# Kernel optimization log

Hardware: AMD Instinct MI355X
Metric: run time of the kernel (lower is better)

Reference implementation:

```python
import jax, jax.numpy as jnp
import numpy as np

H = 16      # num_heads
DK = 128    # head_dim_qk
DV = 128    # head_dim_v
HID = 2048  # hidden_size
KS = 4      # conv kernel size


def _causal_dwconv(x, w, b):
    # x: [B, T, C], w: [C, KS], b: [C] -- depthwise causal conv (torch pads KS-1 then slices [:T])
    xc = jnp.transpose(x, (0, 2, 1))  # [B, C, T]
    out = jax.lax.conv_general_dilated(
        xc, w[:, None, :], window_strides=(1,), padding=[(KS - 1, 0)],
        feature_group_count=xc.shape[1], dimension_numbers=('NCH', 'OIH', 'NCH'))
    out = out + b[None, :, None]
    return jnp.transpose(out, (0, 2, 1))


def setup_inputs() -> dict:
    key = jax.random.key(0)
    ks = jax.random.split(key, 16)
    s = 0.02
    inp = {
        'x':   jax.random.normal(ks[0], (4, 2048, HID), jnp.float32),
        'Wq':  jax.random.normal(ks[1], (HID, H * DK), jnp.float32) * s,
        'Wk':  jax.random.normal(ks[2], (HID, H * DK), jnp.float32) * s,
        'Wv':  jax.random.normal(ks[3], (HID, H * DV), jnp.float32) * s,
        'Wa':  jax.random.normal(ks[4], (HID, H), jnp.float32) * s,
        'ba':  jnp.zeros((H,), jnp.float32),
        'Wb':  jax.random.normal(ks[5], (HID, H), jnp.float32) * s,
        'bb':  jnp.zeros((H,), jnp.float32),
        'Wg':  jax.random.normal(ks[6], (HID, H * DV), jnp.float32) * s,
        'Wo':  jax.random.normal(ks[7], (H * DV, HID), jnp.float32) * s,
        'qcw': jax.random.normal(ks[8], (H * DK, KS), jnp.float32) * 0.3,
        'qcb': jnp.zeros((H * DK,), jnp.float32),
        'kcw': jax.random.normal(ks[9], (H * DK, KS), jnp.float32) * 0.3,
        'kcb': jnp.zeros((H * DK,), jnp.float32),
        'vcw': jax.random.normal(ks[10], (H * DV, KS), jnp.float32) * 0.3,
        'vcb': jnp.zeros((H * DV,), jnp.float32),
        'ln_w': jnp.ones((DV,), jnp.float32),
        'ln_b': jnp.zeros((DV,), jnp.float32),
    }
    return inp


def _forward(x, Wq, Wk, Wv, Wa, ba, Wb, bb, Wg, Wo, qcw, qcb, kcw, kcb, vcw, vcb, ln_w, ln_b):
    B, T, _ = x.shape
    q = jax.nn.silu(_causal_dwconv(x @ Wq, qcw, qcb))
    k = jax.nn.silu(_causal_dwconv(x @ Wk, kcw, kcb))
    v = jax.nn.silu(_causal_dwconv(x @ Wv, vcw, vcb))
    q = q.reshape(B, T, H, DK)
    k = k.reshape(B, T, H, DK) * (DK ** -0.5)
    v = v.reshape(B, T, H, DV)
    alpha = jax.nn.sigmoid(x @ Wa + ba)  # [B, T, H]
    beta = jax.nn.sigmoid(x @ Wb + bb)   # [B, T, H]

    # time-major for scan
    qT = jnp.transpose(q, (1, 0, 2, 3))
    kT = jnp.transpose(k, (1, 0, 2, 3))
    vT = jnp.transpose(v, (1, 0, 2, 3))
    aT = jnp.transpose(alpha, (1, 0, 2))
    bT = jnp.transpose(beta, (1, 0, 2))

    def step(S, inps):
        qt, kt, vt, at, bt = inps
        Sk = jnp.einsum('bhvk,bhk->bhv', S, kt)            # S @ k
        err = Sk - vt
        S = at[..., None, None] * S - bt[..., None, None] * (err[..., None] * kt[:, :, None, :])
        ot = jnp.einsum('bhvk,bhk->bhv', S, qt)            # output uses NEW state
        return S, ot

    S0 = jnp.zeros((B, H, DV, DK), x.dtype)
    _, oT = jax.lax.scan(step, S0, (qT, kT, vT, aT, bT))    # [T, B, H, DV]
    o = jnp.transpose(oT, (1, 0, 2, 3))                      # [B, T, H, DV]

    # LayerNorm over head_dim_v (eps=1e-5)
    mu = jnp.mean(o, axis=-1, keepdims=True)
    var = jnp.mean(jnp.square(o - mu), axis=-1, keepdims=True)
    o = (o - mu) * jax.lax.rsqrt(var + 1e-5) * ln_w + ln_b

    g = jax.nn.sigmoid(x @ Wg).reshape(B, T, H, DV)
    o = (o * g).reshape(B, T, H * DV)
    return o @ Wo


def reference(x, Wq, Wk, Wv, Wa, ba, Wb, bb, Wg, Wo, qcw, qcb, kcw, kcb, vcw, vcb, ln_w, ln_b):
    return _forward(x, Wq, Wk, Wv, Wa, ba, Wb, bb, Wg, Wo, qcw, qcb, kcw, kcb, vcw, vcb, ln_w, ln_b)
```

## Files before the change

### kernel.cpp

```cpp
#include <hip/hip_runtime.h>
#include <stdint.h>

#define H_   16
#define DK_  128
#define DV_  128
#define HID_ 2048
#define KS_  4
#define B_   4
#define T_   2048
#define BT_  (B_*T_)
#define QKVC (3*HID_)
#define C_   32
#define RS_  32

typedef unsigned short u16;
typedef short  bf16x8 __attribute__((ext_vector_type(8)));
typedef u16    u16x8  __attribute__((ext_vector_type(8)));
typedef u16    u16x4  __attribute__((ext_vector_type(4)));
typedef float  f32x4  __attribute__((ext_vector_type(4)));

__device__ __forceinline__ float b2f(u16 u){
  union { unsigned int i; float f; } v; v.i = ((unsigned int)u) << 16; return v.f;
}
__device__ __forceinline__ u16 f2b(float f){
  unsigned int x = __float_as_uint(f);
  unsigned int r = (x + 0x7FFFu + ((x >> 16) & 1u)) >> 16;
  return (u16)r;
}
__device__ __forceinline__ float sigm(float x){ return 1.0f / (1.0f + __expf(-x)); }

#define MFMA16(a,b,c) __builtin_amdgcn_mfma_f32_16x16x32_bf16((a),(b),(c),0,0,0)

__global__ __launch_bounds__(256) void cvt_x_k(const f32x4* __restrict__ src,
                                               u16x4* __restrict__ dst, int n4)
{
  int i0 = blockIdx.x * 256 + threadIdx.x;
  int stride = gridDim.x * 256;
  for (int i = i0; i < n4; i += stride) {
    f32x4 v = src[i];
    u16x4 r; r[0] = f2b(v[0]); r[1] = f2b(v[1]); r[2] = f2b(v[2]); r[3] = f2b(v[3]);
    dst[i] = r;
  }
}

__global__ __launch_bounds__(256) void cvt_small_k(
    const float* __restrict__ qcw, const float* __restrict__ kcw, const float* __restrict__ vcw,
    const float* __restrict__ qcb, const float* __restrict__ kcb, const float* __restrict__ vcb,
    const float* __restrict__ ba,  const float* __restrict__ bb,
    const float* __restrict__ lnw, const float* __restrict__ lnb,
    u16* __restrict__ canon)
{
  int i = blockIdx.x * 256 + threadIdx.x;
  if (i >= 31008) return;
  float v;
  if (i < 24576) {
    const float* s = (i < 8192) ? qcw : (i < 16384) ? kcw : vcw;
    v = s[i & 8191];
  } else if (i < 30720) {
    int j = i - 24576;
    const float* s = (j < 2048) ? qcb : (j < 4096) ? kcb : vcb;
    v = s[j & 2047];
  } else if (i < 30752) {
    int j = i - 30720;
    v = (j < 16) ? ba[j] : bb[j - 16];
  } else {
    int j = i - 30752;
    v = (j < 128) ? lnw[j] : lnb[j - 128];
  }
  canon[i] = f2b(v);
}

__global__ __launch_bounds__(256) void transpose_b(const float* __restrict__ s0,
                                                   const float* __restrict__ s1,
                                                   const float* __restrict__ s2,
                                                   u16* __restrict__ dst,
                                                   int R, int C)
{
  int z = blockIdx.z;
  const float* src = (z == 0) ? s0 : (z == 1) ? s1 : s2;
  u16* d = dst + (size_t)z * R * C;
  __shared__ u16 t[32][33];
  int bx = blockIdx.x * 32;
  int by = blockIdx.y * 32;
  int lx = threadIdx.x & 31, ly = threadIdx.x >> 5;
  #pragma unroll
  for (int i = 0; i < 4; ++i) {
    int r = by + ly + i * 8, c = bx + lx;
    if (r < R && c < C) t[ly + i * 8][lx] = f2b(src[(size_t)r * C + c]);
  }
  __syncthreads();
  #pragma unroll
  for (int i = 0; i < 4; ++i) {
    int r = bx + ly + i * 8;
    int c = by + lx;
    if (r < C && c < R) d[(size_t)r * R + c] = t[lx][ly + i * 8];
  }
}

#define BM 128
#define BN 128
#define BK 32

__device__ __forceinline__ void gload_lds16(const void* gp, void* lp){
  __builtin_amdgcn_global_load_lds(
      (const __attribute__((address_space(1))) void*)gp,
      (__attribute__((address_space(3))) void*)lp, 16, 0, 0);
}

__global__ __launch_bounds__(256) void gemm_bt(const u16* __restrict__ A, int lda,
                                               const u16* __restrict__ Bt, int ldb,
                                               void* __restrict__ C, int ldc,
                                               int K, int out_f32)
{
  __shared__ u16 lsA[BM * BK];
  __shared__ u16 lsB[BN * BK];
  int tid = threadIdx.x, wave = tid >> 6, lane = tid & 63;
  int m0 = blockIdx.y * BM, n0 = blockIdx.x * BN;
  int wm = (wave >> 1) * 64, wn = (wave & 1) * 64;
  int srow = lane >> 2;
  int skel = (lane & 3) * 8;
  int quad = lane >> 4, l16 = lane & 15;

  f32x4 acc[4][4];
  #pragma unroll
  for (int mi = 0; mi < 4; ++mi)
    #pragma unroll
    for (int ni = 0; ni < 4; ++ni)
      #pragma unroll
      for (int r = 0; r < 4; ++r) acc[mi][ni][r] = 0.0f;

  for (int k0 = 0; k0 < K; k0 += BK) {
    __syncthreads();
    #pragma unroll
    for (int i = 0; i < 2; ++i) {
      int row = wave * 32 + i * 16 + srow;
      gload_lds16(A  + (size_t)(m0 + row) * lda + k0 + skel,
                  lsA + (wave * 2048 + i * 1024) / 2);
      gload_lds16(Bt + (size_t)(n0 + row) * ldb + k0 + skel,
                  lsB + (wave * 2048 + i * 1024) / 2);
    }
    __syncthreads();

    const bf16x8* fA = (const bf16x8*)lsA;
    const bf16x8* fB = (const bf16x8*)lsB;
    bf16x8 af[4], bg[4];
    #pragma unroll
    for (int mi = 0; mi < 4; ++mi) af[mi] = fA[(wm + mi * 16 + l16) * 4 + quad];
    #pragma unroll
    for (int ni = 0; ni < 4; ++ni) bg[ni] = fB[(wn + ni * 16 + l16) * 4 + quad];
    #pragma unroll
    for (int mi = 0; mi < 4; ++mi)
      #pragma unroll
      for (int ni = 0; ni < 4; ++ni)
        acc[mi][ni] = MFMA16(af[mi], bg[ni], acc[mi][ni]);
  }

  #pragma unroll
  for (int mi = 0; mi < 4; ++mi)
    #pragma unroll
    for (int ni = 0; ni < 4; ++ni)
      #pragma unroll
      for (int r = 0; r < 4; ++r) {
        int m = m0 + wm + mi * 16 + quad * 4 + r;
        int n = n0 + wn + ni * 16 + l16;
        if (out_f32) ((float*)C)[(size_t)m * ldc + n] = acc[mi][ni][r];
        else         ((u16*)C)[(size_t)m * ldc + n] = f2b(acc[mi][ni][r]);
      }
}

__global__ __launch_bounds__(256) void ab_k(const u16* __restrict__ x,
                                            const u16* __restrict__ WabT,
                                            const u16* __restrict__ ba,
                                            const u16* __restrict__ bb,
                                            float* __restrict__ ab)
{
  int j = threadIdx.x & 31, rl = threadIdx.x >> 5;
  int row = blockIdx.x * 8 + rl;
  const u16x8* xr = (const u16x8*)(x + (size_t)row * HID_);
  const u16x8* wr = (const u16x8*)(WabT + (size_t)j * HID_);
  float acc = 0.f;
  for (int k = 0; k < HID_ / 8; ++k) {
    u16x8 xv = xr[k], wv = wr[k];
    #pragma unroll
    for (int i = 0; i < 8; ++i) acc += b2f(xv[i]) * b2f(wv[i]);
  }
  float bias = (j < 16) ? b2f(ba[j]) : b2f(bb[j - 16]);
  float sg = sigm(acc + bias);
  if (j < 16) ab[(size_t)row * 16 + j] = sg;
  else        ab[(size_t)BT_ * 16 + (size_t)row * 16 + (j - 16)] = sg;
}

__global__ __launch_bounds__(256) void conv_silu_k(const u16* __restrict__ in,
                                                   const u16* __restrict__ cwv,
                                                   const u16* __restrict__ cbv,
                                                   u16* __restrict__ out)
{
  int idx  = blockIdx.x * 256 + threadIdx.x;
  int col8 = idx % (QKVC / 8);
  int t    = idx / (QKVC / 8);
  int col  = col8 * 8;
  int s = col >> 11;

  u16 wl[32];
  #pragma unroll
  for (int i = 0; i < 4; ++i)
    *(u16x8*)(wl + i * 8) = *(const u16x8*)(cwv + (size_t)col * KS_ + i * 8);
  u16x8 bv = *(const u16x8*)(cbv + col);

  float acc[8];
  #pragma unroll
  for (int j = 0; j < 8; ++j) acc[j] = b2f(bv[j]);

  #pragma unroll
  for (int tap = 0; tap < KS_; ++tap) {
    int tt = t - 3 + tap;
    if (tt >= 0) {
      u16x8 xv = *(const u16x8*)(in + (size_t)tt * QKVC + col);
      #pragma unroll
      for (int j = 0; j < 8; ++j) acc[j] = fmaf(b2f(xv[j]), b2f(wl[j * 4 + tap]), acc[j]);
    }
  }
  float scale = (s == 1) ? 0.08838834764831845f : 1.0f;
  u16x8 rv;
  #pragma unroll
  for (int j = 0; j < 8; ++j) {
    float a = acc[j];
    rv[j] = f2b(a * sigm(a) * scale);
  }
  *(u16x8*)(out + (size_t)t * QKVC + col) = rv;
}

__global__ __launch_bounds__(256) void chunk_scan_k(const u16* __restrict__ qkv,
                                                    const float* __restrict__ ab,
                                                    u16* __restrict__ o)
{
  __shared__ __align__(16) char smem[64000];
  u16 (*Kim)[136]  = (u16(*)[136])(smem);
  u16 (*Qim)[136]  = (u16(*)[136])(smem + 8704);
  u16 (*Sh)[136]   = (u16(*)[136])(smem + 17408);
  u16 (*Sl)[136]   = (u16(*)[136])(smem + 26112);
  u16 (*KT)[40]    = (u16(*)[40])(smem + 34816);
  u16 (*Vim)[32]   = (u16(*)[32])(smem + 45056);
  float (*KK)[32]  = (float(*)[32])(smem + 47104);
  float (*KQ)[32]  = (float(*)[32])(smem + 51200);
  float (*SK0)[32] = (float(*)[32])(smem + 55296);
  float (*SQ0)[32] = (float(*)[32])(smem + 59392);
  float (*PL4)[4]  = (float(*)[4])(smem + 63488);
  float (*U)[32]   = (float(*)[32])(smem + 8704);
  u16 (*Gh)[40]  = (u16(*)[40])(smem + 17408);
  u16 (*Gl)[40]  = (u16(*)[40])(smem + 19968);
  u16 (*Uch)[40] = (u16(*)[40])(smem + 22528);
  u16 (*Ucl)[40] = (u16(*)[40])(smem + 25088);
  u16 (*Uth)[40] = (u16(*)[40])(smem + 27648);
  u16 (*Utl)[40] = (u16(*)[40])(smem + 30208);

  int bid = blockIdx.x;
  int chain = bid & 63, rblk = bid >> 6;
  int b = chain >> 4, h = chain & 15;
  int tid = threadIdx.x, wv = tid >> 6, lane = tid & 63;
  int l16 = lane & 15, quad = lane >> 4;

  const u16* kbase = qkv + (size_t)b * T_ * QKVC + HID_ + h * DK_;
  const u16* qbase = qkv + (size_t)b * T_ * QKVC + h * DK_;
  const u16* vbase = qkv + (size_t)b * T_ * QKVC + 2 * HID_ + h * DV_ + rblk * RS_;
  const float* abase = ab + (size_t)b * T_ * 16 + h;
  const float* bbase = abase + (size_t)BT_ * 16;
  u16* obase = o + (size_t)b * T_ * 2048 + h * DV_ + rblk * RS_;

  f32x4 st[2][2];
  #pragma unroll
  for (int rt = 0; rt < 2; ++rt)
    #pragma unroll
    for (int ct = 0; ct < 2; ++ct)
      #pragma unroll
      for (int r = 0; r < 4; ++r) st[rt][ct][r] = 0.f;

  for (int c = 0; c < T_ / C_; ++c) {
    int t0 = c * C_;

    #pragma unroll
    for (int rt = 0; rt < 2; ++rt)
      #pragma unroll
      for (int ct = 0; ct < 2; ++ct)
        #pragma unroll
        for (int r = 0; r < 4; ++r) {
          float s = st[rt][ct][r];
          u16 hi = f2b(s);
          float lo = s - b2f(hi);
          int row = rt * 16 + quad * 4 + r;
          int col = wv * 32 + ct * 16 + l16;
          Sh[row][col] = hi;
          Sl[row][col] = f2b(lo);
        }

    if (wv == 0) {
      float av = (lane < 32) ? abase[(size_t)(t0 + lane) * 16]
                             : bbase[(size_t)(t0 + lane - 32) * 16];
      float p = av;
      #pragma unroll
      for (int d = 1; d < 32; d <<= 1) {
        float up = __shfl_up(p, d);
        if (lane >= d && lane < 32) p *= up;
      }
      float pm1 = __shfl_up(p, 1);
      float bt = __shfl(av, lane + 32);
      if (lane < 32) {
        if (lane == 0) pm1 = 1.f;
        f32x4 g;
        g[0] = bt * pm1;
        g[1] = bt;
        g[2] = 1.0f / p;
        g[3] = p;
        *(f32x4*)PL4[lane] = g;
      }
    } else {
      u16x8 tmp[6];
      int jb = tid - 64;
      #pragma unroll
      for (int it = 0; it < 6; ++it) {
        int j = jb + it * 192;
        if (j < 512) {
          int t = j >> 4, g = j & 15;
          tmp[it] = *(const u16x8*)(kbase + (size_t)(t0 + t) * QKVC + g * 8);
        } else if (j < 1024) {
          int j2 = j - 512; int t = j2 >> 4, g = j2 & 15;
          tmp[it] = *(const u16x8*)(qbase + (size_t)(t0 + t) * QKVC + g * 8);
        } else {
          int j2 = j - 1024; int t = j2 >> 2, rg = j2 & 3;
          tmp[it] = *(const u16x8*)(vbase + (size_t)(t0 + t) * QKVC + rg * 8);
        }
      }
      #pragma unroll
      for (int it = 0; it < 6; ++it) {
        int j = jb + it * 192;
        if (j < 512) {
          int t = j >> 4, g = j & 15;
          *(u16x8*)&Kim[t][g * 8] = tmp[it];
          #pragma unroll
          for (int e = 0; e < 8; ++e) KT[g * 8 + e][t] = tmp[it][e];
        } else if (j < 1024) {
          int j2 = j - 512; int t = j2 >> 4, g = j2 & 15;
          *(u16x8*)&Qim[t][g * 8] = tmp[it];
        } else {
          int j2 = j - 1024; int t = j2 >> 2, rg = j2 & 3;
          *(u16x8*)&Vim[t][rg * 8] = tmp[it];
        }
      }
    }
    __syncthreads();

    {
      int mt = wv >> 1, nt = wv & 1;
      f32x4 aKK = {0.f,0.f,0.f,0.f}, aKQ = {0.f,0.f,0.f,0.f};
      f32x4 aSK = {0.f,0.f,0.f,0.f}, aSQ = {0.f,0.f,0.f,0.f};
      #pragma unroll
      for (int ks = 0; ks < 4; ++ks) {
        bf16x8 Ak  = *(const bf16x8*)&Kim[mt * 16 + l16][ks * 32 + quad * 8];
        bf16x8 Aq  = *(const bf16x8*)&Qim[mt * 16 + l16][ks * 32 + quad * 8];
        bf16x8 Bk  = *(const bf16x8*)&Kim[nt * 16 + l16][ks * 32 + quad * 8];
        bf16x8 Bsh = *(const bf16x8*)&Sh[nt * 16 + l16][ks * 32 + quad * 8];
        bf16x8 Bsl = *(const bf16x8*)&Sl[nt * 16 + l16][ks * 32 + quad * 8];
        aKK = MFMA16(Ak, Bk, aKK);
        aKQ = MFMA16(Aq, Bk, aKQ);
        aSK = MFMA16(Ak, Bsh, aSK);
        aSK = MFMA16(Ak, Bsl, aSK);
        aSQ = MFMA16(Aq, Bsh, aSQ);
        aSQ = MFMA16(Aq, Bsl, aSQ);
      }
      #pragma unroll
      for (int r = 0; r < 4; ++r) {
        int m = mt * 16 + quad * 4 + r, n = nt * 16 + l16;
        KK[m][n] = aKK[r]; KQ[m][n] = aKQ[r];
        SK0[m][n] = aSK[r]; SQ0[m][n] = aSQ[r];
      }
    }
    __syncthreads();

    if (wv == 0 && lane < 32) {
      float ub[C_];
      #pragma unroll
      for (int t = 0; t < C_; ++t) {
        f32x4 g = *(const f32x4*)PL4[t];
        float u = g[0] * SK0[t][lane] - g[1] * b2f(Vim[t][lane]);
        float acc = 0.f;
        #pragma unroll
        for (int i = 0; i < t; ++i) acc = fmaf(KK[t][i], ub[i], acc);
        u = fmaf(-g[0], acc, u);
        U[t][lane] = u;
        ub[t] = g[2] * u;
      }
    }
    __syncthreads();

    {
      float PL31 = PL4[31][3];
      int row = tid & 31, i0 = (tid >> 5) * 4;
      #pragma unroll
      for (int ii = 0; ii < 4; ++ii) {
        int i = i0 + ii;
        float rPi = PL4[i][2];
        float uv = U[i][row];
        u16 h1 = f2b(uv);
        Uth[row][i] = h1; Utl[row][i] = f2b(uv - b2f(h1));
        float ucv = -PL31 * rPi * uv;
        u16 h2 = f2b(ucv);
        Uch[row][i] = h2; Ucl[row][i] = f2b(ucv - b2f(h2));
        float gv = (i <= row) ? (-PL4[row][3] * rPi * KQ[row][i]) : 0.f;
        u16 h3 = f2b(gv);
        Gh[row][i] = h3; Gl[row][i] = f2b(gv - b2f(h3));
      }
    }
    __syncthreads();

    {
      float PL31 = PL4[31][3];
      #pragma unroll
      for (int rt = 0; rt < 2; ++rt) {
        bf16x8 Ah = *(const bf16x8*)&Uch[rt * 16 + l16][quad * 8];
        bf16x8 Al = *(const bf16x8*)&Ucl[rt * 16 + l16][quad * 8];
        #pragma unroll
        for (int ct = 0; ct < 2; ++ct) {
          bf16x8 Bk = *(const bf16x8*)&KT[wv * 32 + ct * 16 + l16][quad * 8];
          f32x4 cacc;
          #pragma unroll
          for (int r = 0; r < 4; ++r) cacc[r] = PL31 * st[rt][ct][r];
          cacc = MFMA16(Ah, Bk, cacc);
          cacc = MFMA16(Al, Bk, cacc);
          st[rt][ct] = cacc;
        }
      }
      int mt = wv >> 1, nt = wv & 1;
      bf16x8 Agh = *(const bf16x8*)&Gh[mt * 16 + l16][quad * 8];
      bf16x8 Agl = *(const bf16x8*)&Gl[mt * 16 + l16][quad * 8];
      bf16x8 Buh = *(const bf16x8*)&Uth[nt * 16 + l16][quad * 8];
      bf16x8 Bul = *(const bf16x8*)&Utl[nt * 16 + l16][quad * 8];
      f32x4 oacc;
      #pragma unroll
      for (int r = 0; r < 4; ++r) {
        int t = mt * 16 + quad * 4 + r;
        oacc[r] = PL4[t][3] * SQ0[t][nt * 16 + l16];
      }
      oacc = MFMA16(Agh, Buh, oacc);
      oacc = MFMA16(Agh, Bul, oacc);
      oacc = MFMA16(Agl, Buh, oacc);
      #pragma unroll
      for (int r = 0; r < 4; ++r) {
        int t = mt * 16 + quad * 4 + r;
        obase[(size_t)(t0 + t) * 2048 + nt * 16 + l16] = f2b(oacc[r]);
      }
    }
    __syncthreads();
  }
}

__global__ __launch_bounds__(256) void ln_gate_k(const u16* __restrict__ o_raw,
                                                 const u16* __restrict__ g,
                                                 const u16* __restrict__ lnw,
                                                 const u16* __restrict__ lnb,
                                                 u16* __restrict__ o_ln)
{
  int gid = blockIdx.x * 4 + (threadIdx.x >> 6);
  int lane = threadIdx.x & 63;
  int row = gid >> 4, h = gid & 15;
  size_t ofs = (size_t)row * 2048 + h * 128 + lane * 2;
  unsigned int e2 = *(const unsigned int*)(o_raw + ofs);
  float ex = b2f((u16)(e2 & 0xffff)), ey = b2f((u16)(e2 >> 16));
  float s = ex + ey, ss = ex * ex + ey * ey;
  #pragma unroll
  for (int m = 1; m < 64; m <<= 1) { s += __shfl_xor(s, m); ss += __shfl_xor(ss, m); }
  float mean = s * (1.f / 128.f);
  float var  = ss * (1.f / 128.f) - mean * mean;
  float rstd = rsqrtf(fmaxf(var, 0.f) + 1e-5f);
  float w0 = b2f(lnw[lane * 2]), w1 = b2f(lnw[lane * 2 + 1]);
  float b0 = b2f(lnb[lane * 2]), b1 = b2f(lnb[lane * 2 + 1]);
  unsigned int g2 = *(const unsigned int*)(g + ofs);
  float g0 = sigm(b2f((u16)(g2 & 0xffff))), g1 = sigm(b2f((u16)(g2 >> 16)));
  float r0 = ((ex - mean) * rstd * w0 + b0) * g0;
  float r1 = ((ey - mean) * rstd * w1 + b1) * g1;
  *(unsigned int*)(o_ln + ofs) = (unsigned int)f2b(r0) | ((unsigned int)f2b(r1) << 16);
}

extern "C" void kernel_launch(void* const* d_in, const int* in_sizes, int n_in,
                              void* d_out, int out_size, void* d_ws, size_t ws_size,
                              hipStream_t stream)
{
  const float* x   = (const float*)d_in[0];
  const float* Wq  = (const float*)d_in[1];
  const float* Wk  = (const float*)d_in[2];
  const float* Wv  = (const float*)d_in[3];
  const float* Wa  = (const float*)d_in[4];
  const float* ba  = (const float*)d_in[5];
  const float* Wb  = (const float*)d_in[6];
  const float* bb  = (const float*)d_in[7];
  const float* Wg  = (const float*)d_in[8];
  const float* Wo  = (const float*)d_in[9];
  const float* qcw = (const float*)d_in[10];
  const float* qcb = (const float*)d_in[11];
  const float* kcw = (const float*)d_in[12];
  const float* kcb = (const float*)d_in[13];
  const float* vcw = (const float*)d_in[14];
  const float* vcb = (const float*)d_in[15];
  const float* lnw = (const float*)d_in[16];
  const float* lnb = (const float*)d_in[17];
  (void)in_sizes; (void)n_in; (void)out_size;

  char* ws = (char*)d_ws;
  size_t off = 0;
  auto alloc = [&](size_t bytes) -> void* {
    void* p = ws + off; off += (bytes + 255) & ~(size_t)255; return p;
  };
  u16* WT    = (u16*)alloc((size_t)3 * HID_ * HID_ * 2);
  u16* WabT  = (u16*)alloc((size_t)32 * HID_ * 2);
  u16* xc    = (u16*)alloc((size_t)BT_ * HID_ * 2);
  u16* canon = (u16*)alloc((size_t)31008 * 2);
  u16* preC  = (u16*)alloc((size_t)BT_ * HID_ * 2 * 2);
  u16* post  = (u16*)alloc((size_t)BT_ * QKVC * 2);
  float* abuf = (float*)alloc((size_t)2 * BT_ * 16 * 4);
  if (off > ws_size) return;

  u16* cw_c  = canon;
  u16* cb_c  = canon + 24576;
  u16* ba_c  = canon + 30720;
  u16* bb_c  = canon + 30736;
  u16* lnw_c = canon + 30752;
  u16* lnb_c = canon + 30880;

  u16* o_raw = preC;
  u16* g_raw = post;
  u16* o_ln  = post + (size_t)BT_ * HID_;
  u16* WTg   = WT;

  dim3 tb(256);

  cvt_x_k<<<dim3(4096), tb, 0, stream>>>((const f32x4*)x, (u16x4*)xc, BT_ * HID_ / 4);
  cvt_small_k<<<dim3(122), tb, 0, stream>>>(qcw, kcw, vcw, qcb, kcb, vcb, ba, bb, lnw, lnb, canon);

  transpose_b<<<dim3(64, 64, 3), tb, 0, stream>>>(Wq, Wk, Wv, WT, HID_, HID_);
  transpose_b<<<dim3(1, 64, 2), tb, 0, stream>>>(Wa, Wb, Wb, WabT, HID_, 16);

  for (int b = 0; b < B_; ++b) {
    const u16* xb = xc + (size_t)b * T_ * HID_;
    gemm_bt<<<dim3(QKVC / BN, T_ / BM), tb, 0, stream>>>(xb, HID_, WT, HID_, preC, QKVC, HID_, 0);
    conv_silu_k<<<dim3(T_ * (QKVC / 8) / 256), tb, 0, stream>>>(
        preC, cw_c, cb_c, post + (size_t)b * T_ * QKVC);
  }

  transpose_b<<<dim3(64, 64, 2), tb, 0, stream>>>(Wg, Wo, Wo, WTg, HID_, HID_);

  ab_k<<<dim3(BT_ / 8), tb, 0, stream>>>(xc, WabT, ba_c, bb_c, abuf);

  chunk_scan_k<<<dim3(256), tb, 0, stream>>>(post, abuf, o_raw);

  gemm_bt<<<dim3(HID_ / BN, BT_ / BM), tb, 0, stream>>>(xc, HID_, WTg, HID_, g_raw, HID_, HID_, 0);

  ln_gate_k<<<dim3(BT_ * H_ / 4), tb, 0, stream>>>(o_raw, g_raw, lnw_c, lnb_c, o_ln);

  gemm_bt<<<dim3(HID_ / BN, BT_ / BM), tb, 0, stream>>>(o_ln, HID_,
      WT + (size_t)HID_ * HID_, HID_, d_out, HID_, HID_, 1);
}
```

Measured before the change: 1.387 ms.

## Split chunk-scan state rows across more blocks and prefetch next chunk

The chunk-scan kernel now gives each block 16 value rows instead of 32, so twice as many blocks (512) run, and shared memory per block shrinks. The next chunk's K/Q/V/alpha-beta loads are issued into registers before the compute of the current chunk, overlapping global latency with work. Intra-chunk matmuls are redistributed by wave, with KK computed only for lower-triangular tiles, G-matrix construction moved into the otherwise idle waves during the sequential solve, and an XOR swizzle added to the K-transpose buffer to cut bank conflicts. The cost is that the KK/KQ and K/Q loads are now repeated in twice as many blocks.

```diff
diff --git a/kernel.cpp b/kernel.cpp
--- a/kernel.cpp
+++ b/kernel.cpp
@@ -11,7 +11,8 @@
 #define BT_  (B_*T_)
 #define QKVC (3*HID_)
 #define C_   32
-#define RS_  32
+#define RS_  16
+#define NC_  (T_/C_)
 
 typedef unsigned short u16;
 typedef short  bf16x8 __attribute__((ext_vector_type(8)));
@@ -234,25 +235,25 @@
                                                     const float* __restrict__ ab,
                                                     u16* __restrict__ o)
 {
-  __shared__ __align__(16) char smem[64000];
+  __shared__ __align__(16) char smem[50688];
   u16 (*Kim)[136]  = (u16(*)[136])(smem);
   u16 (*Qim)[136]  = (u16(*)[136])(smem + 8704);
   u16 (*Sh)[136]   = (u16(*)[136])(smem + 17408);
-  u16 (*Sl)[136]   = (u16(*)[136])(smem + 26112);
-  u16 (*KT)[40]    = (u16(*)[40])(smem + 34816);
-  u16 (*Vim)[32]   = (u16(*)[32])(smem + 45056);
-  float (*KK)[32]  = (float(*)[32])(smem + 47104);
-  float (*KQ)[32]  = (float(*)[32])(smem + 51200);
-  float (*SK0)[32] = (float(*)[32])(smem + 55296);
-  float (*SQ0)[32] = (float(*)[32])(smem + 59392);
-  float (*PL4)[4]  = (float(*)[4])(smem + 63488);
-  float (*U)[32]   = (float(*)[32])(smem + 8704);
-  u16 (*Gh)[40]  = (u16(*)[40])(smem + 17408);
-  u16 (*Gl)[40]  = (u16(*)[40])(smem + 19968);
-  u16 (*Uch)[40] = (u16(*)[40])(smem + 22528);
-  u16 (*Ucl)[40] = (u16(*)[40])(smem + 25088);
-  u16 (*Uth)[40] = (u16(*)[40])(smem + 27648);
-  u16 (*Utl)[40] = (u16(*)[40])(smem + 30208);
+  u16 (*Sl)[136]   = (u16(*)[136])(smem + 21760);
+  u16 (*KT)[40]    = (u16(*)[40])(smem + 26112);
+  u16 (*Vim)[16]   = (u16(*)[16])(smem + 36352);
+  float (*KK)[33]  = (float(*)[33])(smem + 37376);
+  float (*KQ)[33]  = (float(*)[33])(smem + 41600);
+  float (*SK0)[17] = (float(*)[17])(smem + 45824);
+  float (*SQ0)[17] = (float(*)[17])(smem + 48000);
+  float (*PL4)[4]  = (float(*)[4])(smem + 50176);
+  float (*U)[17]   = (float(*)[17])(smem + 8704);
+  u16 (*Uth)[40]   = (u16(*)[40])(smem + 10880);
+  u16 (*Utl)[40]   = (u16(*)[40])(smem + 12160);
+  u16 (*Uch)[40]   = (u16(*)[40])(smem + 13440);
+  u16 (*Ucl)[40]   = (u16(*)[40])(smem + 14720);
+  u16 (*Gh)[40]    = (u16(*)[40])(smem + 17408);
+  u16 (*Gl)[40]    = (u16(*)[40])(smem + 21760);
 
   int bid = blockIdx.x;
   int chain = bid & 63, rblk = bid >> 6;
@@ -267,35 +268,59 @@
   const float* bbase = abase + (size_t)BT_ * 16;
   u16* obase = o + (size_t)b * T_ * 2048 + h * DV_ + rblk * RS_;
 
-  f32x4 st[2][2];
-  #pragma unroll
-  for (int rt = 0; rt < 2; ++rt)
+  f32x4 st[2];
+  #pragma unroll
+  for (int ct = 0; ct < 2; ++ct)
+    #pragma unroll
+    for (int r = 0; r < 4; ++r) st[ct][r] = 0.f;
+
+  int jb = tid - 64;
+  u16x8 stg[6];
+  float avp = 0.f;
+
+  auto LD = [&](int c) {
+    int t0 = c * C_;
+    if (wv == 0) {
+      avp = (lane < 32) ? abase[(size_t)(t0 + lane) * 16]
+                        : bbase[(size_t)(t0 + lane - 32) * 16];
+    } else {
+      #pragma unroll
+      for (int it = 0; it < 6; ++it) {
+        int j = jb + it * 192;
+        if (j < 512) {
+          int t = j >> 4, g = j & 15;
+          stg[it] = *(const u16x8*)(kbase + (size_t)(t0 + t) * QKVC + g * 8);
+        } else if (j < 1024) {
+          int j2 = j - 512, t = j2 >> 4, g = j2 & 15;
+          stg[it] = *(const u16x8*)(qbase + (size_t)(t0 + t) * QKVC + g * 8);
+        } else if (j < 1088) {
+          int j2 = j - 1024, t = j2 >> 1, rg = j2 & 1;
+          stg[it] = *(const u16x8*)(vbase + (size_t)(t0 + t) * QKVC + rg * 8);
+        }
+      }
+    }
+  };
+
+  LD(0);
+
+  for (int c = 0; c < NC_; ++c) {
+    int t0 = c * C_;
+
     #pragma unroll
     for (int ct = 0; ct < 2; ++ct)
       #pragma unroll
-      for (int r = 0; r < 4; ++r) st[rt][ct][r] = 0.f;
-
-  for (int c = 0; c < T_ / C_; ++c) {
-    int t0 = c * C_;
-
-    #pragma unroll
-    for (int rt = 0; rt < 2; ++rt)
-      #pragma unroll
-      for (int ct = 0; ct < 2; ++ct)
-        #pragma unroll
-        for (int r = 0; r < 4; ++r) {
-          float s = st[rt][ct][r];
-          u16 hi = f2b(s);
-          float lo = s - b2f(hi);
-          int row = rt * 16 + quad * 4 + r;
-          int col = wv * 32 + ct * 16 + l16;
-          Sh[row][col] = hi;
-          Sl[row][col] = f2b(lo);
-        }
+      for (int r = 0; r < 4; ++r) {
+        float s = st[ct][r];
+        u16 hi = f2b(s);
+        float lo = s - b2f(hi);
+        int row = quad * 4 + r;
+        int col = wv * 32 + ct * 16 + l16;
+        Sh[row][col] = hi;
+        Sl[row][col] = f2b(lo);
+      }
 
     if (wv == 0) {
-      float av = (lane < 32) ? abase[(size_t)(t0 + lane) * 16]
-                             : bbase[(size_t)(t0 + lane - 32) * 16];
+      float av = avp;
       float p = av;
       #pragma unroll
       for (int d = 1; d < 32; d <<= 1) {
@@ -307,146 +332,173 @@
       if (lane < 32) {
         if (lane == 0) pm1 = 1.f;
         f32x4 g;
-        g[0] = bt * pm1;
-        g[1] = bt;
-        g[2] = 1.0f / p;
-        g[3] = p;
+        g[0] = bt * pm1; g[1] = bt; g[2] = 1.0f / p; g[3] = p;
         *(f32x4*)PL4[lane] = g;
       }
     } else {
-      u16x8 tmp[6];
-      int jb = tid - 64;
       #pragma unroll
       for (int it = 0; it < 6; ++it) {
         int j = jb + it * 192;
         if (j < 512) {
           int t = j >> 4, g = j & 15;
-          tmp[it] = *(const u16x8*)(kbase + (size_t)(t0 + t) * QKVC + g * 8);
+          *(u16x8*)&Kim[t][g * 8] = stg[it];
+          int tb = t >> 3, tl = t & 7;
+          int blk = (tb ^ (g & 3)) << 3;
+          #pragma unroll
+          for (int e = 0; e < 8; ++e)
+            KT[g * 8 + e][blk + tl] = stg[it][e];
         } else if (j < 1024) {
-          int j2 = j - 512; int t = j2 >> 4, g = j2 & 15;
-          tmp[it] = *(const u16x8*)(qbase + (size_t)(t0 + t) * QKVC + g * 8);
-        } else {
-          int j2 = j - 1024; int t = j2 >> 2, rg = j2 & 3;
-          tmp[it] = *(const u16x8*)(vbase + (size_t)(t0 + t) * QKVC + rg * 8);
-        }
-      }
+          int j2 = j - 512, t = j2 >> 4, g = j2 & 15;
+          *(u16x8*)&Qim[t][g * 8] = stg[it];
+        } else if (j < 1088) {
+          int j2 = j - 1024, t = j2 >> 1, rg = j2 & 1;
+          *(u16x8*)&Vim[t][rg * 8] = stg[it];
+        }
+      }
+    }
+    if (c + 1 < NC_) LD(c + 1);
+    __syncthreads();
+
+    if (wv == 0) {
+      #pragma unroll
+      for (int mt = 0; mt < 2; ++mt) {
+        f32x4 acc = {0.f,0.f,0.f,0.f};
+        #pragma unroll
+        for (int ks = 0; ks < 4; ++ks) {
+          bf16x8 A  = *(const bf16x8*)&Kim[mt * 16 + l16][ks * 32 + quad * 8];
+          bf16x8 Bh = *(const bf16x8*)&Sh[l16][ks * 32 + quad * 8];
+          bf16x8 Bl = *(const bf16x8*)&Sl[l16][ks * 32 + quad * 8];
+          acc = MFMA16(A, Bh, acc);
+          acc = MFMA16(A, Bl, acc);
+        }
+        #pragma unroll
+        for (int r = 0; r < 4; ++r) SK0[mt * 16 + quad * 4 + r][l16] = acc[r];
+      }
+    } else if (wv == 1) {
+      const int mts[3] = {0, 1, 1}, nts[3] = {0, 0, 1};
+      #pragma unroll
+      for (int jj = 0; jj < 3; ++jj) {
+        int mt = mts[jj], nt = nts[jj];
+        f32x4 acc = {0.f,0.f,0.f,0.f};
+        #pragma unroll
+        for (int ks = 0; ks < 4; ++ks) {
+          bf16x8 A = *(const bf16x8*)&Kim[mt * 16 + l16][ks * 32 + quad * 8];
+          bf16x8 B = *(const bf16x8*)&Kim[nt * 16 + l16][ks * 32 + quad * 8];
+          acc = MFMA16(A, B, acc);
+        }
+        #pragma unroll
+        for (int r = 0; r < 4; ++r) KK[mt * 16 + quad * 4 + r][nt * 16 + l16] = acc[r];
+      }
+    } else {
+      int nt = wv - 2;
+      #pragma unroll
+      for (int mt = 0; mt < 2; ++mt) {
+        f32x4 acc = {0.f,0.f,0.f,0.f};
+        #pragma unroll
+        for (int ks = 0; ks < 4; ++ks) {
+          bf16x8 A = *(const bf16x8*)&Qim[mt * 16 + l16][ks * 32 + quad * 8];
+          bf16x8 B = *(const bf16x8*)&Kim[nt * 16 + l16][ks * 32 + quad * 8];
+          acc = MFMA16(A, B, acc);
+        }
+        #pragma unroll
+        for (int r = 0; r < 4; ++r) KQ[mt * 16 + quad * 4 + r][nt * 16 + l16] = acc[r];
+      }
+      int mt = nt;
+      f32x4 acc = {0.f,0.f,0.f,0.f};
+      #pragma unroll
+      for (int ks = 0; ks < 4; ++ks) {
+        bf16x8 A  = *(const bf16x8*)&Qim[mt * 16 + l16][ks * 32 + quad * 8];
+        bf16x8 Bh = *(const bf16x8*)&Sh[l16][ks * 32 + quad * 8];
+        bf16x8 Bl = *(const bf16x8*)&Sl[l16][ks * 32 + quad * 8];
+        acc = MFMA16(A, Bh, acc);
+        acc = MFMA16(A, Bl, acc);
+      }
+      #pragma unroll
+      for (int r = 0; r < 4; ++r) SQ0[mt * 16 + quad * 4 + r][l16] = acc[r];
+    }
+    __syncthreads();
+
+    if (wv == 0) {
+      if (lane < 16) {
+        float ub[C_];
+        #pragma unroll
+        for (int t = 0; t < C_; ++t) {
+          f32x4 g = *(const f32x4*)PL4[t];
+          float u = g[0] * SK0[t][lane] - g[1] * b2f(Vim[t][lane]);
+          float acc = 0.f;
+          #pragma unroll
+          for (int i = 0; i < t; ++i) acc = fmaf(KK[t][i], ub[i], acc);
+          u = fmaf(-g[0], acc, u);
+          U[t][lane] = u;
+          ub[t] = g[2] * u;
+        }
+      }
+    } else {
       #pragma unroll
       for (int it = 0; it < 6; ++it) {
-        int j = jb + it * 192;
-        if (j < 512) {
-          int t = j >> 4, g = j & 15;
-          *(u16x8*)&Kim[t][g * 8] = tmp[it];
-          #pragma unroll
-          for (int e = 0; e < 8; ++e) KT[g * 8 + e][t] = tmp[it][e];
-        } else if (j < 1024) {
-          int j2 = j - 512; int t = j2 >> 4, g = j2 & 15;
-          *(u16x8*)&Qim[t][g * 8] = tmp[it];
-        } else {
-          int j2 = j - 1024; int t = j2 >> 2, rg = j2 & 3;
-          *(u16x8*)&Vim[t][rg * 8] = tmp[it];
-        }
-      }
-    }
-    __syncthreads();
-
-    {
-      int mt = wv >> 1, nt = wv & 1;
-      f32x4 aKK = {0.f,0.f,0.f,0.f}, aKQ = {0.f,0.f,0.f,0.f};
-      f32x4 aSK = {0.f,0.f,0.f,0.f}, aSQ = {0.f,0.f,0.f,0.f};
-      #pragma unroll
-      for (int ks = 0; ks < 4; ++ks) {
-        bf16x8 Ak  = *(const bf16x8*)&Kim[mt * 16 + l16][ks * 32 + quad * 8];
-        bf16x8 Aq  = *(const bf16x8*)&Qim[mt * 16 + l16][ks * 32 + quad * 8];
-        bf16x8 Bk  = *(const bf16x8*)&Kim[nt * 16 + l16][ks * 32 + quad * 8];
-        bf16x8 Bsh = *(const bf16x8*)&Sh[nt * 16 + l16][ks * 32 + quad * 8];
-        bf16x8 Bsl = *(const bf16x8*)&Sl[nt * 16 + l16][ks * 32 + quad * 8];
-        aKK = MFMA16(Ak, Bk, aKK);
-        aKQ = MFMA16(Aq, Bk, aKQ);
-        aSK = MFMA16(Ak, Bsh, aSK);
-        aSK = MFMA16(Ak, Bsl, aSK);
-        aSQ = MFMA16(Aq, Bsh, aSQ);
-        aSQ = MFMA16(Aq, Bsl, aSQ);
-      }
-      #pragma unroll
-      for (int r = 0; r < 4; ++r) {
-        int m = mt * 16 + quad * 4 + r, n = nt * 16 + l16;
-        KK[m][n] = aKK[r]; KQ[m][n] = aKQ[r];
-        SK0[m][n] = aSK[r]; SQ0[m][n] = aSQ[r];
-      }
-    }
-    __syncthreads();
-
-    if (wv == 0 && lane < 32) {
-      float ub[C_];
-      #pragma unroll
-      for (int t = 0; t < C_; ++t) {
-        f32x4 g = *(const f32x4*)PL4[t];
-        float u = g[0] * SK0[t][lane] - g[1] * b2f(Vim[t][lane]);
-        float acc = 0.f;
-        #pragma unroll
-        for (int i = 0; i < t; ++i) acc = fmaf(KK[t][i], ub[i], acc);
-        u = fmaf(-g[0], acc, u);
-        U[t][lane] = u;
-        ub[t] = g[2] * u;
+        int idx = jb + it * 192;
+        if (idx < 1024) {
+          int t = idx >> 5, i = idx & 31;
+          float gv = (i <= t) ? (-PL4[t][3] * PL4[i][2] * KQ[t][i]) : 0.f;
+          u16 hh = f2b(gv);
+          Gh[t][i] = hh;
+          Gl[t][i] = f2b(gv - b2f(hh));
+        }
       }
     }
     __syncthreads();
 
     {
       float PL31 = PL4[31][3];
-      int row = tid & 31, i0 = (tid >> 5) * 4;
-      #pragma unroll
-      for (int ii = 0; ii < 4; ++ii) {
-        int i = i0 + ii;
-        float rPi = PL4[i][2];
+      #pragma unroll
+      for (int e = 0; e < 2; ++e) {
+        int idx = tid * 2 + e;
+        int row = idx & 15, i = idx >> 4;
         float uv = U[i][row];
         u16 h1 = f2b(uv);
         Uth[row][i] = h1; Utl[row][i] = f2b(uv - b2f(h1));
-        float ucv = -PL31 * rPi * uv;
+        float ucv = -PL31 * PL4[i][2] * uv;
         u16 h2 = f2b(ucv);
         Uch[row][i] = h2; Ucl[row][i] = f2b(ucv - b2f(h2));
-        float gv = (i <= row) ? (-PL4[row][3] * rPi * KQ[row][i]) : 0.f;
-        u16 h3 = f2b(gv);
-        Gh[row][i] = h3; Gl[row][i] = f2b(gv - b2f(h3));
       }
     }
     __syncthreads();
 
     {
       float PL31 = PL4[31][3];
-      #pragma unroll
-      for (int rt = 0; rt < 2; ++rt) {
-        bf16x8 Ah = *(const bf16x8*)&Uch[rt * 16 + l16][quad * 8];
-        bf16x8 Al = *(const bf16x8*)&Ucl[rt * 16 + l16][quad * 8];
-        #pragma unroll
-        for (int ct = 0; ct < 2; ++ct) {
-          bf16x8 Bk = *(const bf16x8*)&KT[wv * 32 + ct * 16 + l16][quad * 8];
-          f32x4 cacc;
-          #pragma unroll
-          for (int r = 0; r < 4; ++r) cacc[r] = PL31 * st[rt][ct][r];
-          cacc = MFMA16(Ah, Bk, cacc);
-          cacc = MFMA16(Al, Bk, cacc);
-          st[rt][ct] = cacc;
-        }
-      }
-      int mt = wv >> 1, nt = wv & 1;
-      bf16x8 Agh = *(const bf16x8*)&Gh[mt * 16 + l16][quad * 8];
-      bf16x8 Agl = *(const bf16x8*)&Gl[mt * 16 + l16][quad * 8];
-      bf16x8 Buh = *(const bf16x8*)&Uth[nt * 16 + l16][quad * 8];
-      bf16x8 Bul = *(const bf16x8*)&Utl[nt * 16 + l16][quad * 8];
-      f32x4 oacc;
-      #pragma unroll
-      for (int r = 0; r < 4; ++r) {
-        int t = mt * 16 + quad * 4 + r;
-        oacc[r] = PL4[t][3] * SQ0[t][nt * 16 + l16];
-      }
-      oacc = MFMA16(Agh, Buh, oacc);
-      oacc = MFMA16(Agh, Bul, oacc);
-      oacc = MFMA16(Agl, Buh, oacc);
-      #pragma unroll
-      for (int r = 0; r < 4; ++r) {
-        int t = mt * 16 + quad * 4 + r;
-        obase[(size_t)(t0 + t) * 2048 + nt * 16 + l16] = f2b(oacc[r]);
+      bf16x8 Ah = *(const bf16x8*)&Uch[l16][quad * 8];
+      bf16x8 Al = *(const bf16x8*)&Ucl[l16][quad * 8];
+      #pragma unroll
+      for (int ct = 0; ct < 2; ++ct) {
+        int col = wv * 32 + ct * 16 + l16;
+        bf16x8 Bk = *(const bf16x8*)&KT[col][(quad ^ ((col >> 3) & 3)) << 3];
+        f32x4 cacc;
+        #pragma unroll
+        for (int r = 0; r < 4; ++r) cacc[r] = PL31 * st[ct][r];
+        cacc = MFMA16(Ah, Bk, cacc);
+        cacc = MFMA16(Al, Bk, cacc);
+        st[ct] = cacc;
+      }
+      if (wv < 2) {
+        int mt = wv;
+        bf16x8 Agh = *(const bf16x8*)&Gh[mt * 16 + l16][quad * 8];
+        bf16x8 Agl = *(const bf16x8*)&Gl[mt * 16 + l16][quad * 8];
+        bf16x8 Buh = *(const bf16x8*)&Uth[l16][quad * 8];
+        bf16x8 Bul = *(const bf16x8*)&Utl[l16][quad * 8];
+        f32x4 oacc;
+        #pragma unroll
+        for (int r = 0; r < 4; ++r) {
+          int t = mt * 16 + quad * 4 + r;
+          oacc[r] = PL4[t][3] * SQ0[t][l16];
+        }
+        oacc = MFMA16(Agh, Buh, oacc);
+        oacc = MFMA16(Agh, Bul, oacc);
+        oacc = MFMA16(Agl, Buh, oacc);
+        #pragma unroll
+        for (int r = 0; r < 4; ++r) {
+          int t = mt * 16 + quad * 4 + r;
+          obase[(size_t)(t0 + t) * 2048 + l16] = f2b(oacc[r]);
+        }
       }
     }
     __syncthreads();
@@ -549,7 +601,7 @@
 
   ab_k<<<dim3(BT_ / 8), tb, 0, stream>>>(xc, WabT, ba_c, bb_c, abuf);
 
-  chunk_scan_k<<<dim3(256), tb, 0, stream>>>(post, abuf, o_raw);
+  chunk_scan_k<<<dim3(512), tb, 0, stream>>>(post, abuf, o_raw);
 
   gemm_bt<<<dim3(HID_ / BN, BT_ / BM), tb, 0, stream>>>(xc, HID_, WTg, HID_, g_raw, HID_, HID_, 0);
 
```

Result: slower. 1.638 ms (+18.1%).
